# Kernel optimization log

Hardware: AMD Instinct MI355X
Metric: run time of the kernel (lower is better)

Reference implementation:

```python
import jax, jax.numpy as jnp
import numpy as np
import math

B, S, D = 4, 1024, 1024
E, DE = 8, 128            # n_experts, expert_dim (D == E*DE)
TOPK = 2
SCALE = 1.0 / math.sqrt(D)  # source divides by sqrt(self.dim) = sqrt(transformer_dim)


def setup_inputs() -> dict:
    key = jax.random.key(0)
    k1, k2, k3, k4, k5 = jax.random.split(key, 5)
    Q = jax.random.normal(k1, (B, S, D), dtype=jnp.float32)
    K = jax.random.normal(k2, (B, S, D), dtype=jnp.float32)
    V = jax.random.normal(k3, (B, S, D), dtype=jnp.float32)
    route_prob = jax.random.uniform(k4, (B, E), dtype=jnp.float32)
    # first-stage MoE dispatch (idx_list): expert_mask[e, b] == 1 iff batch b routed to expert e
    expert_mask = jax.random.randint(k5, (E, B), 0, 2).astype(jnp.int32)
    mask = jnp.ones((B, S), dtype=jnp.float32)  # accepted but unused by the source forward
    return {"Q": Q, "K": K, "V": V, "route_prob": route_prob,
            "expert_mask": expert_mask, "mask": mask}


def reference(Q, K, V, route_prob, expert_mask, mask):
    # RowParallelMatmulWithMoE: each expert e attends using its 128-wide feature slice
    Qe = Q.reshape(B, S, E, DE)
    Ke = K.reshape(B, S, E, DE)
    scores = jnp.einsum('bsed,bted->ebst', Qe, Ke) * SCALE   # [E, B, S, S]
    probs = jax.nn.softmax(scores, axis=-1)                   # per-expert softmax (dropout p=0)
    # index_add_ scatter: sum routed experts' attention maps per batch element
    m1 = expert_mask.astype(Q.dtype)                          # [E, B]
    attn = jnp.einsum('eb,ebst->bst', m1, probs)              # [B, S, S]
    # preprocess: top-k expert re-selection from route_prob -> new idx_list
    _, top_idx = jax.lax.top_k(route_prob, TOPK)              # [B, TOPK]
    m2 = jnp.zeros((B, E), dtype=Q.dtype).at[jnp.arange(B)[:, None], top_idx].set(1.0)
    # ColumnParallelMatmulWithMoE: attn @ V restricted to each selected expert's V slice
    Ve = V.reshape(B, S, E, DE)
    out = jnp.einsum('bst,bted->bsed', attn, Ve) * m2[:, None, :, None]  # [B, S, E, DE]
    return out.reshape(B, S, D)
```

## Files before the change

kernel.cpp:

```cpp
#include <hip/hip_runtime.h>
#include <hip/hip_bf16.h>
#include <stdint.h>

#define B_ 4
#define S_ 1024
#define D_ 1024
#define E_ 8
#define DE_ 128
#define SCALE_ 0.03125f

typedef __attribute__((ext_vector_type(8))) short short8;
typedef __attribute__((ext_vector_type(4))) float f32x4;
typedef unsigned short ushort_t;
typedef unsigned int uint32;

__device__ __forceinline__ ushort_t f2bf(float f) {
    uint32 u = __float_as_uint(f);
    uint32 r = u + 0x7fffu + ((u >> 16) & 1u);
    return (ushort_t)(r >> 16);
}

#define GLOAD_LDS16(g, l) __builtin_amdgcn_global_load_lds( \
    (const __attribute__((address_space(1))) unsigned int*)(g), \
    (__attribute__((address_space(3))) unsigned int*)(l), 16, 0, 0)

__device__ __forceinline__ void stage64(const ushort_t* __restrict__ g,
                                        size_t stride, ushort_t* lds,
                                        int w, int lane) {
    #pragma unroll
    for (int j = 0; j < 4; ++j) {
        int cb = (w * 4 + j) << 6;
        int ch = cb + lane;
        int r = ch >> 4, c = ch & 15;
        GLOAD_LDS16(g + (size_t)r * stride + ((c ^ (r & 7)) << 3),
                    lds + ((size_t)cb << 3));
    }
}
__device__ __forceinline__ void stage128(const ushort_t* __restrict__ g,
                                         size_t stride, ushort_t* lds,
                                         int w, int lane) {
    #pragma unroll
    for (int j = 0; j < 8; ++j) {
        int cb = (w * 8 + j) << 6;
        int ch = cb + lane;
        int r = ch >> 4, c = ch & 15;
        GLOAD_LDS16(g + (size_t)r * stride + ((c ^ (r & 7)) << 3),
                    lds + ((size_t)cb << 3));
    }
}
__device__ __forceinline__ short8 fld(const ushort_t* lds, int row, int c) {
    return *(const short8*)(lds + (((row << 4) + (c ^ (row & 7))) << 3));
}

__device__ __forceinline__ void top2(const float* rp, int& i1, int& i2) {
    float v1 = rp[0]; i1 = 0;
    #pragma unroll
    for (int i = 1; i < 8; ++i) { float v = rp[i]; if (v > v1) { v1 = v; i1 = i; } }
    float v2 = -1e30f; i2 = 0;
    #pragma unroll
    for (int i = 0; i < 8; ++i) {
        if (i == i1) continue;
        float v = rp[i]; if (v > v2) { v2 = v; i2 = i; }
    }
}

__global__ __launch_bounds__(256) void prep_kernel(
        const float* __restrict__ Q, const float* __restrict__ K,
        const float* __restrict__ V, const float* __restrict__ route,
        const int* __restrict__ em,
        ushort_t* __restrict__ Qb, ushort_t* __restrict__ Kb,
        ushort_t* __restrict__ Vt) {
    __shared__ ushort_t tile[64][130];
    const int tid = threadIdx.x;
    const int sc = blockIdx.x, e = blockIdx.y, b = blockIdx.z;
    const int s0 = sc * 64;
    const size_t plane = ((size_t)(b * 8 + e)) << 17;

    const bool ak = em[e * B_ + b] != 0;
    int i1, i2; top2(route + b * 8, i1, i2);
    const bool av = (e == i1) || (e == i2);
    if (!ak && !av) return;

    if (ak) {
        #pragma unroll
        for (int i = 0; i < 8; ++i) {
            int idx = tid + i * 256, r = idx >> 5, c4 = idx & 31;
            size_t in_off = ((size_t)(b * 1024 + s0 + r) << 10) + (e << 7) + (c4 << 2);
            float4 q = *(const float4*)(Q + in_off);
            float4 k = *(const float4*)(K + in_off);
            size_t oo = plane + (((size_t)(s0 + r)) << 7) + (c4 << 2);
            *(ushort4*)(Qb + oo) = make_ushort4(f2bf(q.x), f2bf(q.y), f2bf(q.z), f2bf(q.w));
            *(ushort4*)(Kb + oo) = make_ushort4(f2bf(k.x), f2bf(k.y), f2bf(k.z), f2bf(k.w));
        }
    }
    if (av) {
        #pragma unroll
        for (int i = 0; i < 8; ++i) {
            int idx = tid + i * 256, r = idx >> 5, c4 = idx & 31;
            size_t in_off = ((size_t)(b * 1024 + s0 + r) << 10) + (e << 7) + (c4 << 2);
            float4 v = *(const float4*)(V + in_off);
            ushort_t* p = &tile[r][c4 << 2];
            p[0] = f2bf(v.x); p[1] = f2bf(v.y); p[2] = f2bf(v.z); p[3] = f2bf(v.w);
        }
        __syncthreads();
        #pragma unroll
        for (int i = 0; i < 4; ++i) {
            int item = tid + i * 256, d = item & 127, sg = item >> 7;
            union { uint4 q; ushort_t u[8]; } tmp;
            #pragma unroll
            for (int j = 0; j < 8; ++j) tmp.u[j] = tile[sg * 8 + j][d];
            *(uint4*)(Vt + plane + (((size_t)d) << 10) + s0 + (sg << 3)) = tmp.q;
        }
    }
}

__global__ __launch_bounds__(256, 2) void attn_pass1(
        const ushort_t* __restrict__ Qb, const ushort_t* __restrict__ Kb,
        const int* __restrict__ em, float* __restrict__ lsums) {

    __shared__ __align__(16) ushort_t qtile[64 * 128];
    __shared__ __align__(16) ushort_t ktile[128 * 128];
    __shared__ float red[2][64];

    const int stile = blockIdx.x, e = blockIdx.y, b = blockIdx.z;
    if (em[e * B_ + b] == 0) return;

    const int tid = threadIdx.x;
    const int w = tid >> 6, lane = tid & 63;
    const int quad = lane >> 4, l16 = lane & 15;
    const int wm = w & 1, wn = w >> 1;
    const int s0 = stile * 64;
    const size_t plane = ((size_t)(b * 8 + e)) << 17;

    stage64(Qb + plane + ((size_t)s0 << 7), 128, qtile, w, lane);
    stage128(Kb + plane, 128, ktile, w, lane);
    __syncthreads();

    short8 af[2][4];
    #pragma unroll
    for (int mi = 0; mi < 2; ++mi)
        #pragma unroll
        for (int kk = 0; kk < 4; ++kk)
            af[mi][kk] = fld(qtile, 32 * wm + 16 * mi + l16, (kk << 2) + quad);

    float rsum[2][4] = {{0.f,0.f,0.f,0.f},{0.f,0.f,0.f,0.f}};

    for (int tc = 0; tc < 8; ++tc) {
        f32x4 sacc[2][4];
        #pragma unroll
        for (int mi = 0; mi < 2; ++mi)
            #pragma unroll
            for (int ni = 0; ni < 4; ++ni) sacc[mi][ni] = (f32x4){0.f,0.f,0.f,0.f};
        #pragma unroll
        for (int ni = 0; ni < 4; ++ni)
            #pragma unroll
            for (int kk = 0; kk < 4; ++kk) {
                short8 bf = fld(ktile, 64 * wn + 16 * ni + l16, (kk << 2) + quad);
                #pragma unroll
                for (int mi = 0; mi < 2; ++mi)
                    sacc[mi][ni] = __builtin_amdgcn_mfma_f32_16x16x32_bf16(
                        af[mi][kk], bf, sacc[mi][ni], 0, 0, 0);
            }
        #pragma unroll
        for (int mi = 0; mi < 2; ++mi)
            #pragma unroll
            for (int ni = 0; ni < 4; ++ni)
                #pragma unroll
                for (int r = 0; r < 4; ++r)
                    rsum[mi][r] += __expf(sacc[mi][ni][r] * SCALE_);
        __syncthreads();
        if (tc < 7)
            stage128(Kb + plane + (((size_t)(tc + 1)) << 14), 128, ktile, w, lane);
        __syncthreads();
    }

    #pragma unroll
    for (int off = 1; off < 16; off <<= 1)
        #pragma unroll
        for (int mi = 0; mi < 2; ++mi)
            #pragma unroll
            for (int r = 0; r < 4; ++r)
                rsum[mi][r] += __shfl_xor(rsum[mi][r], off, 64);
    if (l16 == 0) {
        #pragma unroll
        for (int mi = 0; mi < 2; ++mi)
            #pragma unroll
            for (int r = 0; r < 4; ++r)
                red[wn][32 * wm + 16 * mi + quad * 4 + r] = rsum[mi][r];
    }
    __syncthreads();
    if (tid < 64)
        lsums[(((size_t)(b * 8 + e)) << 10) + s0 + tid] = red[0][tid] + red[1][tid];
}

__global__ __launch_bounds__(256, 2) void attn_passC(
        const ushort_t* __restrict__ Qb, const ushort_t* __restrict__ Kb,
        const float* __restrict__ lsums, const int* __restrict__ em,
        ushort_t* __restrict__ attnB) {

    __shared__ __align__(16) ushort_t qtile[64 * 128];
    __shared__ __align__(16) ushort_t ktile[128 * 128];

    const int stile = blockIdx.x, tt = blockIdx.y, b = blockIdx.z;
    const int tid = threadIdx.x;
    const int w = tid >> 6, lane = tid & 63;
    const int quad = lane >> 4, l16 = lane & 15;
    const int wm = w & 1, wn = w >> 1;
    const int s0 = stile * 64, t0 = tt * 128;

    f32x4 aacc[2][4];
    #pragma unroll
    for (int mi = 0; mi < 2; ++mi)
        #pragma unroll
        for (int ni = 0; ni < 4; ++ni) aacc[mi][ni] = (f32x4){0.f,0.f,0.f,0.f};

    for (int e = 0; e < 8; ++e) {
        if (em[e * B_ + b] == 0) continue;
        const size_t plane = ((size_t)(b * 8 + e)) << 17;

        stage64(Qb + plane + ((size_t)s0 << 7), 128, qtile, w, lane);
        stage128(Kb + plane + ((size_t)t0 << 7), 128, ktile, w, lane);
        __syncthreads();

        float rinv[2][4];
        #pragma unroll
        for (int mi = 0; mi < 2; ++mi)
            #pragma unroll
            for (int r = 0; r < 4; ++r)
                rinv[mi][r] = 1.0f / lsums[(((size_t)(b * 8 + e)) << 10)
                                           + s0 + 32 * wm + 16 * mi + quad * 4 + r];

        short8 af[2][4];
        #pragma unroll
        for (int mi = 0; mi < 2; ++mi)
            #pragma unroll
            for (int kk = 0; kk < 4; ++kk)
                af[mi][kk] = fld(qtile, 32 * wm + 16 * mi + l16, (kk << 2) + quad);

        f32x4 sacc[2][4];
        #pragma unroll
        for (int mi = 0; mi < 2; ++mi)
            #pragma unroll
            for (int ni = 0; ni < 4; ++ni) sacc[mi][ni] = (f32x4){0.f,0.f,0.f,0.f};
        #pragma unroll
        for (int ni = 0; ni < 4; ++ni)
            #pragma unroll
            for (int kk = 0; kk < 4; ++kk) {
                short8 bf = fld(ktile, 64 * wn + 16 * ni + l16, (kk << 2) + quad);
                #pragma unroll
                for (int mi = 0; mi < 2; ++mi)
                    sacc[mi][ni] = __builtin_amdgcn_mfma_f32_16x16x32_bf16(
                        af[mi][kk], bf, sacc[mi][ni], 0, 0, 0);
            }
        #pragma unroll
        for (int mi = 0; mi < 2; ++mi)
            #pragma unroll
            for (int ni = 0; ni < 4; ++ni)
                #pragma unroll
                for (int r = 0; r < 4; ++r)
                    aacc[mi][ni][r] += __expf(sacc[mi][ni][r] * SCALE_) * rinv[mi][r];
        __syncthreads();
    }

    #pragma unroll
    for (int mi = 0; mi < 2; ++mi)
        #pragma unroll
        for (int ni = 0; ni < 4; ++ni)
            #pragma unroll
            for (int r = 0; r < 4; ++r)
                attnB[(((size_t)(b * 1024 + s0 + 32 * wm + 16 * mi + quad * 4 + r)) << 10)
                      + t0 + 64 * wn + 16 * ni + l16] = f2bf(aacc[mi][ni][r]);
}

__global__ __launch_bounds__(256, 2) void attn_pass2(
        const ushort_t* __restrict__ Vt, const ushort_t* __restrict__ attnB,
        const float* __restrict__ route, float* __restrict__ out) {

    __shared__ __align__(16) ushort_t atile[64 * 128];
    __shared__ __align__(16) ushort_t vtile[128 * 128];

    const int stile = blockIdx.x, e = blockIdx.y, b = blockIdx.z;
    const int tid = threadIdx.x;
    const int w = tid >> 6, lane = tid & 63;
    const int quad = lane >> 4, l16 = lane & 15;
    const int wm = w & 1, wn = w >> 1;
    const int s0 = stile * 64;

    int i1, i2; top2(route + b * 8, i1, i2);

    if (e != i1 && e != i2) {
        #pragma unroll
        for (int i = 0; i < 8; ++i) {
            int idx = tid + i * 256, r = idx >> 5, c4 = idx & 31;
            *(float4*)(out + (((size_t)(b * 1024 + s0 + r)) << 10) + (e << 7) + (c4 << 2))
                = make_float4(0.f, 0.f, 0.f, 0.f);
        }
        return;
    }

    const size_t vplane = ((size_t)(b * 8 + e)) << 17;
    const ushort_t* abase = attnB + (((size_t)(b * 1024 + s0)) << 10);

    f32x4 oacc[2][4];
    #pragma unroll
    for (int mi = 0; mi < 2; ++mi)
        #pragma unroll
        for (int ni = 0; ni < 4; ++ni) oacc[mi][ni] = (f32x4){0.f,0.f,0.f,0.f};

    for (int tc = 0; tc < 8; ++tc) {
        stage64(abase + (tc << 7), 1024, atile, w, lane);
        stage128(Vt + vplane + (tc << 7), 1024, vtile, w, lane);
        __syncthreads();

        short8 af[2][4];
        #pragma unroll
        for (int mi = 0; mi < 2; ++mi)
            #pragma unroll
            for (int kk = 0; kk < 4; ++kk)
                af[mi][kk] = fld(atile, 32 * wm + 16 * mi + l16, (kk << 2) + quad);
        #pragma unroll
        for (int ni = 0; ni < 4; ++ni)
            #pragma unroll
            for (int kk = 0; kk < 4; ++kk) {
                short8 bf = fld(vtile, 64 * wn + 16 * ni + l16, (kk << 2) + quad);
                #pragma unroll
                for (int mi = 0; mi < 2; ++mi)
                    oacc[mi][ni] = __builtin_amdgcn_mfma_f32_16x16x32_bf16(
                        af[mi][kk], bf, oacc[mi][ni], 0, 0, 0);
            }
        __syncthreads();
    }

    #pragma unroll
    for (int mi = 0; mi < 2; ++mi)
        #pragma unroll
        for (int ni = 0; ni < 4; ++ni)
            #pragma unroll
            for (int r = 0; r < 4; ++r)
                out[(((size_t)(b * 1024 + s0 + 32 * wm + 16 * mi + quad * 4 + r)) << 10)
                    + (e << 7) + 64 * wn + 16 * ni + l16] = oacc[mi][ni][r];
}

extern "C" void kernel_launch(void* const* d_in, const int* in_sizes, int n_in,
                              void* d_out, int out_size, void* d_ws, size_t ws_size,
                              hipStream_t stream) {
    const float* Q     = (const float*)d_in[0];
    const float* K     = (const float*)d_in[1];
    const float* V     = (const float*)d_in[2];
    const float* route = (const float*)d_in[3];
    const int*   em    = (const int*)d_in[4];
    float* out = (float*)d_out;

    const size_t NB = (size_t)B_ * E_ * S_ * DE_;
    ushort_t* Qb = (ushort_t*)d_ws;
    ushort_t* Kb = Qb + NB;
    ushort_t* Vt = Kb + NB;
    float*    lsums = (float*)(Vt + NB);
    ushort_t* attnB = (ushort_t*)(lsums + (size_t)B_ * E_ * S_);

    dim3 gp(16, 8, 4);
    prep_kernel<<<gp, 256, 0, stream>>>(Q, K, V, route, em, Qb, Kb, Vt);
    dim3 g1(16, 8, 4);
    attn_pass1<<<g1, 256, 0, stream>>>(Qb, Kb, em, lsums);
    dim3 gc(16, 8, 4);
    attn_passC<<<gc, 256, 0, stream>>>(Qb, Kb, lsums, em, attnB);
    dim3 g2(16, 8, 4);
    attn_pass2<<<g2, 256, 0, stream>>>(Vt, attnB, route, out);
}
```

Baseline: 139.3 us.

## Double-buffer LDS tiles across all three attention passes and shrink passC tiles

Adds double-buffered shared-memory staging in pass1, passC and pass2, so the next K, Q/K or attn/V tile is loaded while the current one is being computed, and drops one barrier per iteration. PassC switches to 64-wide t tiles with a doubled grid and a precomputed packed list of active experts. Pass2's LDS roughly doubles to about 96KB, so launch bounds drop to one block per CU, which lowers occupancy. The goal is to hide global-to-LDS latency at the cost of more shared memory and smaller per-block MFMA tiles.

```diff
diff --git a/kernel.cpp b/kernel.cpp
--- a/kernel.cpp
+++ b/kernel.cpp
@@ -119,7 +119,7 @@
         const int* __restrict__ em, float* __restrict__ lsums) {
 
     __shared__ __align__(16) ushort_t qtile[64 * 128];
-    __shared__ __align__(16) ushort_t ktile[128 * 128];
+    __shared__ __align__(16) ushort_t ktile[2][64 * 128];
     __shared__ float red[2][64];
 
     const int stile = blockIdx.x, e = blockIdx.y, b = blockIdx.z;
@@ -133,7 +133,7 @@
     const size_t plane = ((size_t)(b * 8 + e)) << 17;
 
     stage64(Qb + plane + ((size_t)s0 << 7), 128, qtile, w, lane);
-    stage128(Kb + plane, 128, ktile, w, lane);
+    stage64(Kb + plane, 128, ktile[0], w, lane);
     __syncthreads();
 
     short8 af[2][4];
@@ -145,17 +145,22 @@
 
     float rsum[2][4] = {{0.f,0.f,0.f,0.f},{0.f,0.f,0.f,0.f}};
 
-    for (int tc = 0; tc < 8; ++tc) {
-        f32x4 sacc[2][4];
-        #pragma unroll
-        for (int mi = 0; mi < 2; ++mi)
-            #pragma unroll
-            for (int ni = 0; ni < 4; ++ni) sacc[mi][ni] = (f32x4){0.f,0.f,0.f,0.f};
-        #pragma unroll
-        for (int ni = 0; ni < 4; ++ni)
+    for (int tc = 0; tc < 16; ++tc) {
+        if (tc < 15)
+            stage64(Kb + plane + (((size_t)(tc + 1)) << 13), 128,
+                    ktile[(tc + 1) & 1], w, lane);
+        const ushort_t* kb = ktile[tc & 1];
+
+        f32x4 sacc[2][2];
+        #pragma unroll
+        for (int mi = 0; mi < 2; ++mi)
+            #pragma unroll
+            for (int ni = 0; ni < 2; ++ni) sacc[mi][ni] = (f32x4){0.f,0.f,0.f,0.f};
+        #pragma unroll
+        for (int ni = 0; ni < 2; ++ni)
             #pragma unroll
             for (int kk = 0; kk < 4; ++kk) {
-                short8 bf = fld(ktile, 64 * wn + 16 * ni + l16, (kk << 2) + quad);
+                short8 bf = fld(kb, 32 * wn + 16 * ni + l16, (kk << 2) + quad);
                 #pragma unroll
                 for (int mi = 0; mi < 2; ++mi)
                     sacc[mi][ni] = __builtin_amdgcn_mfma_f32_16x16x32_bf16(
@@ -164,13 +169,10 @@
         #pragma unroll
         for (int mi = 0; mi < 2; ++mi)
             #pragma unroll
-            for (int ni = 0; ni < 4; ++ni)
+            for (int ni = 0; ni < 2; ++ni)
                 #pragma unroll
                 for (int r = 0; r < 4; ++r)
                     rsum[mi][r] += __expf(sacc[mi][ni][r] * SCALE_);
-        __syncthreads();
-        if (tc < 7)
-            stage128(Kb + plane + (((size_t)(tc + 1)) << 14), 128, ktile, w, lane);
         __syncthreads();
     }
 
@@ -198,86 +200,103 @@
         const float* __restrict__ lsums, const int* __restrict__ em,
         ushort_t* __restrict__ attnB) {
 
-    __shared__ __align__(16) ushort_t qtile[64 * 128];
-    __shared__ __align__(16) ushort_t ktile[128 * 128];
+    __shared__ __align__(16) ushort_t qtile[2][64 * 128];
+    __shared__ __align__(16) ushort_t ktile[2][64 * 128];
 
     const int stile = blockIdx.x, tt = blockIdx.y, b = blockIdx.z;
     const int tid = threadIdx.x;
     const int w = tid >> 6, lane = tid & 63;
     const int quad = lane >> 4, l16 = lane & 15;
     const int wm = w & 1, wn = w >> 1;
-    const int s0 = stile * 64, t0 = tt * 128;
-
-    f32x4 aacc[2][4];
-    #pragma unroll
-    for (int mi = 0; mi < 2; ++mi)
-        #pragma unroll
-        for (int ni = 0; ni < 4; ++ni) aacc[mi][ni] = (f32x4){0.f,0.f,0.f,0.f};
-
-    for (int e = 0; e < 8; ++e) {
-        if (em[e * B_ + b] == 0) continue;
-        const size_t plane = ((size_t)(b * 8 + e)) << 17;
-
-        stage64(Qb + plane + ((size_t)s0 << 7), 128, qtile, w, lane);
-        stage128(Kb + plane + ((size_t)t0 << 7), 128, ktile, w, lane);
+    const int s0 = stile * 64, t0 = tt * 64;
+
+    uint32 epack = 0; int ne = 0;
+    #pragma unroll
+    for (int e = 0; e < 8; ++e)
+        if (em[e * B_ + b] != 0) { epack |= (uint32)e << (3 * ne); ++ne; }
+
+    f32x4 aacc[2][2];
+    #pragma unroll
+    for (int mi = 0; mi < 2; ++mi)
+        #pragma unroll
+        for (int ni = 0; ni < 2; ++ni) aacc[mi][ni] = (f32x4){0.f,0.f,0.f,0.f};
+
+    if (ne > 0) {
+        {
+            int e0 = epack & 7;
+            size_t pl = ((size_t)(b * 8 + e0)) << 17;
+            stage64(Qb + pl + ((size_t)s0 << 7), 128, qtile[0], w, lane);
+            stage64(Kb + pl + ((size_t)t0 << 7), 128, ktile[0], w, lane);
+        }
         __syncthreads();
 
-        float rinv[2][4];
-        #pragma unroll
-        for (int mi = 0; mi < 2; ++mi)
-            #pragma unroll
-            for (int r = 0; r < 4; ++r)
-                rinv[mi][r] = 1.0f / lsums[(((size_t)(b * 8 + e)) << 10)
-                                           + s0 + 32 * wm + 16 * mi + quad * 4 + r];
-
-        short8 af[2][4];
-        #pragma unroll
-        for (int mi = 0; mi < 2; ++mi)
-            #pragma unroll
-            for (int kk = 0; kk < 4; ++kk)
-                af[mi][kk] = fld(qtile, 32 * wm + 16 * mi + l16, (kk << 2) + quad);
-
-        f32x4 sacc[2][4];
-        #pragma unroll
-        for (int mi = 0; mi < 2; ++mi)
-            #pragma unroll
-            for (int ni = 0; ni < 4; ++ni) sacc[mi][ni] = (f32x4){0.f,0.f,0.f,0.f};
-        #pragma unroll
-        for (int ni = 0; ni < 4; ++ni)
-            #pragma unroll
-            for (int kk = 0; kk < 4; ++kk) {
-                short8 bf = fld(ktile, 64 * wn + 16 * ni + l16, (kk << 2) + quad);
-                #pragma unroll
-                for (int mi = 0; mi < 2; ++mi)
-                    sacc[mi][ni] = __builtin_amdgcn_mfma_f32_16x16x32_bf16(
-                        af[mi][kk], bf, sacc[mi][ni], 0, 0, 0);
+        for (int i = 0; i < ne; ++i) {
+            if (i + 1 < ne) {
+                int en = (epack >> (3 * (i + 1))) & 7;
+                size_t pl = ((size_t)(b * 8 + en)) << 17;
+                stage64(Qb + pl + ((size_t)s0 << 7), 128, qtile[(i + 1) & 1], w, lane);
+                stage64(Kb + pl + ((size_t)t0 << 7), 128, ktile[(i + 1) & 1], w, lane);
             }
-        #pragma unroll
-        for (int mi = 0; mi < 2; ++mi)
-            #pragma unroll
-            for (int ni = 0; ni < 4; ++ni)
+            int e = (epack >> (3 * i)) & 7;
+            float rinv[2][4];
+            #pragma unroll
+            for (int mi = 0; mi < 2; ++mi)
                 #pragma unroll
                 for (int r = 0; r < 4; ++r)
-                    aacc[mi][ni][r] += __expf(sacc[mi][ni][r] * SCALE_) * rinv[mi][r];
-        __syncthreads();
-    }
-
-    #pragma unroll
-    for (int mi = 0; mi < 2; ++mi)
-        #pragma unroll
-        for (int ni = 0; ni < 4; ++ni)
+                    rinv[mi][r] = 1.0f / lsums[(((size_t)(b * 8 + e)) << 10)
+                                               + s0 + 32 * wm + 16 * mi + quad * 4 + r];
+
+            const ushort_t* qb = qtile[i & 1];
+            const ushort_t* kb = ktile[i & 1];
+            short8 af[2][4];
+            #pragma unroll
+            for (int mi = 0; mi < 2; ++mi)
+                #pragma unroll
+                for (int kk = 0; kk < 4; ++kk)
+                    af[mi][kk] = fld(qb, 32 * wm + 16 * mi + l16, (kk << 2) + quad);
+
+            f32x4 sacc[2][2];
+            #pragma unroll
+            for (int mi = 0; mi < 2; ++mi)
+                #pragma unroll
+                for (int ni = 0; ni < 2; ++ni) sacc[mi][ni] = (f32x4){0.f,0.f,0.f,0.f};
+            #pragma unroll
+            for (int ni = 0; ni < 2; ++ni)
+                #pragma unroll
+                for (int kk = 0; kk < 4; ++kk) {
+                    short8 bf = fld(kb, 32 * wn + 16 * ni + l16, (kk << 2) + quad);
+                    #pragma unroll
+                    for (int mi = 0; mi < 2; ++mi)
+                        sacc[mi][ni] = __builtin_amdgcn_mfma_f32_16x16x32_bf16(
+                            af[mi][kk], bf, sacc[mi][ni], 0, 0, 0);
+                }
+            #pragma unroll
+            for (int mi = 0; mi < 2; ++mi)
+                #pragma unroll
+                for (int ni = 0; ni < 2; ++ni)
+                    #pragma unroll
+                    for (int r = 0; r < 4; ++r)
+                        aacc[mi][ni][r] += __expf(sacc[mi][ni][r] * SCALE_) * rinv[mi][r];
+            __syncthreads();
+        }
+    }
+
+    #pragma unroll
+    for (int mi = 0; mi < 2; ++mi)
+        #pragma unroll
+        for (int ni = 0; ni < 2; ++ni)
             #pragma unroll
             for (int r = 0; r < 4; ++r)
                 attnB[(((size_t)(b * 1024 + s0 + 32 * wm + 16 * mi + quad * 4 + r)) << 10)
-                      + t0 + 64 * wn + 16 * ni + l16] = f2bf(aacc[mi][ni][r]);
-}
-
-__global__ __launch_bounds__(256, 2) void attn_pass2(
+                      + t0 + 32 * wn + 16 * ni + l16] = f2bf(aacc[mi][ni][r]);
+}
+
+__global__ __launch_bounds__(256, 1) void attn_pass2(
         const ushort_t* __restrict__ Vt, const ushort_t* __restrict__ attnB,
         const float* __restrict__ route, float* __restrict__ out) {
 
-    __shared__ __align__(16) ushort_t atile[64 * 128];
-    __shared__ __align__(16) ushort_t vtile[128 * 128];
+    __shared__ __align__(16) ushort_t atile[2][64 * 128];
+    __shared__ __align__(16) ushort_t vtile[2][128 * 128];
 
     const int stile = blockIdx.x, e = blockIdx.y, b = blockIdx.z;
     const int tid = threadIdx.x;
@@ -301,6 +320,10 @@
     const size_t vplane = ((size_t)(b * 8 + e)) << 17;
     const ushort_t* abase = attnB + (((size_t)(b * 1024 + s0)) << 10);
 
+    stage64(abase, 1024, atile[0], w, lane);
+    stage128(Vt + vplane, 1024, vtile[0], w, lane);
+    __syncthreads();
+
     f32x4 oacc[2][4];
     #pragma unroll
     for (int mi = 0; mi < 2; ++mi)
@@ -308,21 +331,24 @@
         for (int ni = 0; ni < 4; ++ni) oacc[mi][ni] = (f32x4){0.f,0.f,0.f,0.f};
 
     for (int tc = 0; tc < 8; ++tc) {
-        stage64(abase + (tc << 7), 1024, atile, w, lane);
-        stage128(Vt + vplane + (tc << 7), 1024, vtile, w, lane);
-        __syncthreads();
+        if (tc < 7) {
+            stage64(abase + ((tc + 1) << 7), 1024, atile[(tc + 1) & 1], w, lane);
+            stage128(Vt + vplane + ((tc + 1) << 7), 1024, vtile[(tc + 1) & 1], w, lane);
+        }
+        const ushort_t* at = atile[tc & 1];
+        const ushort_t* vt = vtile[tc & 1];
 
         short8 af[2][4];
         #pragma unroll
         for (int mi = 0; mi < 2; ++mi)
             #pragma unroll
             for (int kk = 0; kk < 4; ++kk)
-                af[mi][kk] = fld(atile, 32 * wm + 16 * mi + l16, (kk << 2) + quad);
+                af[mi][kk] = fld(at, 32 * wm + 16 * mi + l16, (kk << 2) + quad);
         #pragma unroll
         for (int ni = 0; ni < 4; ++ni)
             #pragma unroll
             for (int kk = 0; kk < 4; ++kk) {
-                short8 bf = fld(vtile, 64 * wn + 16 * ni + l16, (kk << 2) + quad);
+                short8 bf = fld(vt, 64 * wn + 16 * ni + l16, (kk << 2) + quad);
                 #pragma unroll
                 for (int mi = 0; mi < 2; ++mi)
                     oacc[mi][ni] = __builtin_amdgcn_mfma_f32_16x16x32_bf16(
@@ -362,7 +388,7 @@
     prep_kernel<<<gp, 256, 0, stream>>>(Q, K, V, route, em, Qb, Kb, Vt);
     dim3 g1(16, 8, 4);
     attn_pass1<<<g1, 256, 0, stream>>>(Qb, Kb, em, lsums);
-    dim3 gc(16, 8, 4);
+    dim3 gc(16, 16, 4);
     attn_passC<<<gc, 256, 0, stream>>>(Qb, Kb, lsums, em, attnB);
     dim3 g2(16, 8, 4);
     attn_pass2<<<g2, 256, 0, stream>>>(Vt, attnB, route, out);
```

Result: slower. 149.5 us (+7.4%).
